# Kernel tuning notes

Hardware: AMD Instinct MI355X
Metric: run time of the kernel (lower is better)

The kernel has to match this reference:

```python
import jax, jax.numpy as jnp
import numpy as np

B, S, D, H = 4, 2048, 512, 8
DK = D // H
EPS = 1e-5


def setup_inputs() -> dict:
    key = jax.random.key(0)
    ks = jax.random.split(key, 9)
    inp = {
        "input_Q": jax.random.normal(ks[0], (B, S, D), jnp.float32),
        "input_K": jax.random.normal(ks[1], (B, S, D), jnp.float32),
        "input_V": jax.random.normal(ks[2], (B, S, D), jnp.float32),
        # causal mask: True = masked (upper triangle above diagonal)
        "attn_mask": jnp.broadcast_to(
            jnp.triu(jnp.ones((S, S), jnp.bool_), k=1), (B, S, S)
        ),
        # nn.Linear weights (torch stores [out, in]; y = x @ W.T)
        "Wq": jax.random.normal(ks[3], (D, D), jnp.float32) / np.sqrt(D),
        "Wk": jax.random.normal(ks[4], (D, D), jnp.float32) / np.sqrt(D),
        "Wv": jax.random.normal(ks[5], (D, D), jnp.float32) / np.sqrt(D),
        "Wo": jax.random.normal(ks[6], (D, D), jnp.float32) / np.sqrt(D),
        "gamma": jnp.ones((D,), jnp.float32),
        "beta": jnp.zeros((D,), jnp.float32),
    }
    return inp


def _layer_norm(x, gamma, beta):
    mu = jnp.mean(x, axis=-1, keepdims=True)
    var = jnp.mean(jnp.square(x - mu), axis=-1, keepdims=True)
    return (x - mu) * jax.lax.rsqrt(var + EPS) * gamma + beta


def reference(input_Q, input_K, input_V, attn_mask, Wq, Wk, Wv, Wo, gamma, beta):
    # projections: [B,S,D] -> [B,H,S,DK]
    def split_heads(x):
        return x.reshape(x.shape[0], x.shape[1], H, DK).transpose(0, 2, 1, 3)

    Q = split_heads(input_Q @ Wq.T)
    K = split_heads(input_K @ Wk.T)
    V = split_heads(input_V @ Wv.T)

    # scores: [B,H,Sq,Sk], explicit materialization as in the original
    scores = jnp.einsum("bhqd,bhkd->bhqk", Q, K) / np.sqrt(DK).astype(np.float32)
    scores = jnp.where(attn_mask[:, None, :, :], -jnp.inf, scores)
    attn = jax.nn.softmax(scores, axis=-1)
    context = jnp.einsum("bhqk,bhkd->bhqd", attn, V)  # [B,H,Sq,DK]

    context = context.transpose(0, 2, 1, 3).reshape(input_Q.shape[0], -1, D)
    output = context @ Wo.T
    out = _layer_norm(output + input_Q, gamma, beta)
    return (out, attn)
```

## Files before the change

kernel.cpp:

```cpp
#include <hip/hip_runtime.h>

typedef unsigned short u16;
typedef __bf16 bf16x8 __attribute__((ext_vector_type(8)));
typedef float f32x4 __attribute__((ext_vector_type(4)));
typedef unsigned short u16x4 __attribute__((ext_vector_type(4)));

#define MFMA_B16(a, b, c) __builtin_amdgcn_mfma_f32_16x16x32_bf16((a), (b), (c), 0, 0, 0)

__device__ __forceinline__ u16 f2bf(float f) {
  unsigned int u = __float_as_uint(f);
  u += 0x7FFFu + ((u >> 16) & 1u);
  return (u16)(u >> 16);
}

__device__ __forceinline__ u16x4 f4_to_bf4(float4 v) {
  u16x4 r;
  r[0] = f2bf(v.x); r[1] = f2bf(v.y); r[2] = f2bf(v.z); r[3] = f2bf(v.w);
  return r;
}

__global__ __launch_bounds__(256) void cvt3(const float* __restrict__ a,
                                            const float* __restrict__ b,
                                            const float* __restrict__ c,
                                            u16* __restrict__ dst, int n4, int n) {
  int i = blockIdx.x * 256 + threadIdx.x;
  int stride = gridDim.x * 256;
  const float4* a4 = (const float4*)a;
  const float4* b4 = (const float4*)b;
  const float4* c4 = (const float4*)c;
  u16x4* d0 = (u16x4*)dst;
  u16x4* d1 = (u16x4*)(dst + (size_t)n);
  u16x4* d2 = (u16x4*)(dst + (size_t)2 * n);
  for (; i < n4; i += stride) {
    d0[i] = f4_to_bf4(a4[i]);
    d1[i] = f4_to_bf4(b4[i]);
    d2[i] = f4_to_bf4(c4[i]);
  }
}

__global__ __launch_bounds__(256) void cvtW(const float* __restrict__ a,
                                            const float* __restrict__ b,
                                            const float* __restrict__ c,
                                            const float* __restrict__ d,
                                            u16* __restrict__ dst, int n4, int n) {
  int i = blockIdx.x * 256 + threadIdx.x;
  int stride = gridDim.x * 256;
  const float4* a4 = (const float4*)a;
  const float4* b4 = (const float4*)b;
  const float4* c4 = (const float4*)c;
  const float4* d4 = (const float4*)d;
  u16x4* o0 = (u16x4*)dst;
  u16x4* o1 = (u16x4*)(dst + (size_t)n);
  u16x4* o2 = (u16x4*)(dst + (size_t)2 * n);
  u16x4* o3 = (u16x4*)(dst + (size_t)3 * n);
  for (; i < n4; i += stride) {
    o0[i] = f4_to_bf4(a4[i]);
    o1[i] = f4_to_bf4(b4[i]);
    o2[i] = f4_to_bf4(c4[i]);
    o3[i] = f4_to_bf4(d4[i]);
  }
}

template <bool OUT_F32>
__device__ __forceinline__ void gemm_body(const u16* __restrict__ A,
                                          const u16* __restrict__ Bw,
                                          u16* __restrict__ Cb, float* __restrict__ Cf,
                                          int bm, int bn) {
  __shared__ __align__(16) u16 As[128][40];
  __shared__ __align__(16) u16 Bs[128][40];
  const int tid = threadIdx.x;
  const int wave = tid >> 6, lane = tid & 63;
  const int g = lane >> 4, l16 = lane & 15;
  const int wr = (wave >> 1) * 64, wc = (wave & 1) * 64;
  const int srow = tid >> 1, scol = (tid & 1) * 16;
  const u16* Ar = A + (size_t)(bm + srow) * 512 + scol;
  const u16* Br = Bw + (size_t)(bn + srow) * 512 + scol;
  f32x4 acc[4][4] = {};
  for (int k0 = 0; k0 < 512; k0 += 32) {
    *(uint4*)(&As[srow][scol])     = *(const uint4*)(Ar + k0);
    *(uint4*)(&As[srow][scol + 8]) = *(const uint4*)(Ar + k0 + 8);
    *(uint4*)(&Bs[srow][scol])     = *(const uint4*)(Br + k0);
    *(uint4*)(&Bs[srow][scol + 8]) = *(const uint4*)(Br + k0 + 8);
    __syncthreads();
    bf16x8 af[4], bfr[4];
#pragma unroll
    for (int i = 0; i < 4; ++i) af[i] = *(const bf16x8*)(&As[wr + i * 16 + l16][g * 8]);
#pragma unroll
    for (int j = 0; j < 4; ++j) bfr[j] = *(const bf16x8*)(&Bs[wc + j * 16 + l16][g * 8]);
#pragma unroll
    for (int i = 0; i < 4; ++i)
#pragma unroll
      for (int j = 0; j < 4; ++j)
        acc[i][j] = MFMA_B16(af[i], bfr[j], acc[i][j]);
    __syncthreads();
  }
#pragma unroll
  for (int i = 0; i < 4; ++i)
#pragma unroll
    for (int j = 0; j < 4; ++j)
#pragma unroll
      for (int r = 0; r < 4; ++r) {
        int row = bm + wr + i * 16 + g * 4 + r;
        int col = bn + wc + j * 16 + l16;
        if constexpr (OUT_F32)
          Cf[(size_t)row * 512 + col] = acc[i][j][r];
        else
          Cb[(size_t)row * 512 + col] = f2bf(acc[i][j][r]);
      }
}

__global__ __launch_bounds__(256) void gemm_qkv(const u16* __restrict__ Xbf,
                                                const u16* __restrict__ Wbf,
                                                u16* __restrict__ QKVp) {
  int z = blockIdx.z;
  gemm_body<false>(Xbf + (size_t)z * 4194304, Wbf + (size_t)z * 262144,
                   QKVp + (size_t)z * 4194304, nullptr,
                   blockIdx.x * 128, blockIdx.y * 128);
}

__global__ __launch_bounds__(256) void gemm_f32out(const u16* __restrict__ A,
                                                   const u16* __restrict__ Bw,
                                                   float* __restrict__ C) {
  gemm_body<true>(A, Bw, nullptr, C, blockIdx.x * 128, blockIdx.y * 128);
}

__global__ __launch_bounds__(256) void transpose_v(const u16* __restrict__ Vp,
                                                   u16* __restrict__ Vt) {
  __shared__ __align__(16) u16 t[64][72];
  const int b = blockIdx.z;
  const int s0 = blockIdx.x * 64, d0 = blockIdx.y * 64;
  const u16* in = Vp + (size_t)b * 2048 * 512;
  u16* outp = Vt + (size_t)b * 512 * 2048;
  const int tid = threadIdx.x;
  const int r = tid >> 2;
  const int c = (tid & 3) * 16;
  const uint4* src = (const uint4*)(in + (size_t)(s0 + r) * 512 + d0 + c);
  uint4 v0 = src[0], v1 = src[1];
  *(uint4*)(&t[r][c]) = v0;
  *(uint4*)(&t[r][c + 8]) = v1;
  __syncthreads();
  u16 tmp[16];
#pragma unroll
  for (int j = 0; j < 16; ++j) tmp[j] = t[c + j][r];
  uint4* dst = (uint4*)(outp + (size_t)(d0 + r) * 2048 + s0 + c);
  dst[0] = *(uint4*)(&tmp[0]);
  dst[1] = *(uint4*)(&tmp[8]);
}

__global__ __launch_bounds__(512, 2) void lsum_kernel(const u16* __restrict__ Qp,
                                                      const u16* __restrict__ Kp,
                                                      float* __restrict__ invl) {
  __shared__ __align__(16) u16 Ks[2][8192];
  const int tid = threadIdx.x;
  const int wave = tid >> 6, lane = tid & 63;
  const int g = lane >> 4, l16 = lane & 15;
  const int id = blockIdx.x;
  const int xcd = id & 7;
  const int r = id >> 3;
  const int bh = xcd * 4 + (r & 3);
  const int p = r >> 2;
  const int strip = wave >> 2;
  const int pw = wave & 3;
  const int nktH = 16 - p, nktL = p + 1;
  const int myNkt = strip ? nktL : nktH;
  const int myBase = (strip ? p : 15 - p) * 128 + pw * 32;
  const int b = bh >> 3, h = bh & 7;
  const char* KhB = (const char*)Kp + (size_t)b * 2097152 + h * 128;
  const u16* Qh = Qp + (size_t)b * 1048576 + h * 64;
  char* KsC = (char*)Ks;

  const int sr_r = tid >> 2;
  const int sr_c = (tid & 3) * 2;
  const size_t sr_src = (size_t)sr_r * 1024 + sr_c * 16;
  const int sr_d0 = sr_r * 128 + ((sr_c ^ (sr_r & 7)) << 4);
  const int sr_d1 = sr_r * 128 + (((sr_c + 1) ^ (sr_r & 7)) << 4);
  uint4 sr[2];

#define STAGE_LOAD(KT)                                                         \
  { sr[0] = *(const uint4*)(KhB + (size_t)(KT) * 131072 + sr_src);             \
    sr[1] = *(const uint4*)(KhB + (size_t)(KT) * 131072 + sr_src + 16); }
#define STAGE_WRITE(CUR)                                                       \
  { *(uint4*)(KsC + (CUR) * 16384 + sr_d0) = sr[0];                            \
    *(uint4*)(KsC + (CUR) * 16384 + sr_d1) = sr[1]; }
#define BAR_READS_DONE()                                                       \
  { asm volatile("" ::: "memory");                                             \
    __builtin_amdgcn_s_barrier();                                              \
    __builtin_amdgcn_sched_barrier(0); }
#define BAR_WRITES_VISIBLE()                                                   \
  { asm volatile("s_waitcnt lgkmcnt(0)" ::: "memory");                         \
    __builtin_amdgcn_sched_barrier(0);                                         \
    __builtin_amdgcn_s_barrier();                                              \
    __builtin_amdgcn_sched_barrier(0); }

  const int qrow0 = myBase + l16;
  const int qrow1 = myBase + 16 + l16;
  bf16x8 q00 = *(const bf16x8*)(Qh + (size_t)qrow0 * 512 + g * 8);
  bf16x8 q01 = *(const bf16x8*)(Qh + (size_t)qrow0 * 512 + 32 + g * 8);
  bf16x8 q10 = *(const bf16x8*)(Qh + (size_t)qrow1 * 512 + g * 8);
  bf16x8 q11 = *(const bf16x8*)(Qh + (size_t)qrow1 * 512 + 32 + g * 8);

  float ls0 = 0.f, ls1 = 0.f;
  STAGE_LOAD(0); STAGE_WRITE(0);
  if (nktH > 1) STAGE_LOAD(1);
  BAR_WRITES_VISIBLE();
  int cur = 0;
  for (int kt = 0; kt < nktH; ++kt) {
    const int ktb = kt * 128;
    const bool act = (kt < myNkt);
    const bool dg = (kt == myNkt - 1);
    const char* Kc = KsC + cur * 16384;
    if (act) {
#pragma unroll
      for (int kf = 0; kf < 8; ++kf) {
        const int ro = (kf * 16 + l16) * 128;
        bf16x8 ka = *(const bf16x8*)(Kc + ro + ((g ^ (l16 & 7)) << 4));
        bf16x8 kb = *(const bf16x8*)(Kc + ro + (((4 + g) ^ (l16 & 7)) << 4));
        const int kbase = ktb + kf * 16 + g * 4;
        f32x4 c0 = {0.f, 0.f, 0.f, 0.f};
        f32x4 c1 = {0.f, 0.f, 0.f, 0.f};
        __builtin_amdgcn_s_setprio(1);
        c0 = MFMA_B16(ka, q00, c0);
        c0 = MFMA_B16(kb, q01, c0);
        c1 = MFMA_B16(ka, q10, c1);
        c1 = MFMA_B16(kb, q11, c1);
        __builtin_amdgcn_s_setprio(0);
        if (dg) {
#pragma unroll
          for (int rr = 0; rr < 4; ++rr) {
            ls0 += (kbase + rr > qrow0) ? 0.f : __expf(c0[rr] * 0.125f);
            ls1 += (kbase + rr > qrow1) ? 0.f : __expf(c1[rr] * 0.125f);
          }
        } else {
          ls0 += __expf(c0[0] * 0.125f) + __expf(c0[1] * 0.125f)
               + __expf(c0[2] * 0.125f) + __expf(c0[3] * 0.125f);
          ls1 += __expf(c1[0] * 0.125f) + __expf(c1[1] * 0.125f)
               + __expf(c1[2] * 0.125f) + __expf(c1[3] * 0.125f);
        }
      }
    }
    if (kt + 1 < nktH) {
      BAR_READS_DONE();
      STAGE_WRITE(cur ^ 1);
      if (kt + 2 < nktH) STAGE_LOAD(kt + 2);
      BAR_WRITES_VISIBLE();
      cur ^= 1;
    }
  }
  ls0 += __shfl_xor(ls0, 16); ls0 += __shfl_xor(ls0, 32);
  ls1 += __shfl_xor(ls1, 16); ls1 += __shfl_xor(ls1, 32);
  if (lane < 16) {
    invl[(size_t)bh * 2048 + qrow0] = 1.f / ls0;
    invl[(size_t)bh * 2048 + qrow1] = 1.f / ls1;
  }
#undef STAGE_LOAD
#undef STAGE_WRITE
#undef BAR_READS_DONE
#undef BAR_WRITES_VISIBLE
}

__global__ __launch_bounds__(512, 4) void attn_kernel(const u16* __restrict__ Qp,
                                                      const u16* __restrict__ Kp,
                                                      const u16* __restrict__ Vt,
                                                      const float* __restrict__ invl,
                                                      float* __restrict__ attn_all,
                                                      u16* __restrict__ ctx) {
  __shared__ __align__(16) u16 Ks[2][8192];
  __shared__ __align__(16) u16 Plds[8][16][128];
  const int tid = threadIdx.x;
  const int wave = tid >> 6, lane = tid & 63;
  const int g = lane >> 4, l16 = lane & 15;
  const int strip = wave >> 2;
  const int pw = wave & 3;
  const int id = blockIdx.x;
  const int r8 = id >> 3;
  const int bh = (id & 7) * 4 + (r8 & 3);
  const int pair = r8 >> 2;
  const int sLo = pair, sHi = 31 - pair;
  const int b = bh >> 3, h = bh & 7;
  const int nktH = sHi / 2 + 1, nktL = sLo / 2 + 1;
  const int myNkt = strip ? nktL : nktH;
  const int myS = strip ? sLo : sHi;
  const char* KhB = (const char*)Kp + (size_t)b * 2097152 + h * 128;
  const char* VhB = (const char*)Vt + ((size_t)b * 512 + h * 64) * 4096;
  const u16* Qh = Qp + (size_t)b * 1048576 + h * 64;
  float* attn = attn_all + (size_t)bh * 4194304;
  char* KsC = (char*)Ks;
  char* Pw = (char*)&Plds[wave][0][0];
  const int swk = (l16 & 7) << 4;

  const int sr_r = tid >> 2;
  const int sr_c = (tid & 3) * 2;
  const size_t sr_src = (size_t)sr_r * 1024 + sr_c * 16;
  const int sr_d0 = sr_r * 128 + ((sr_c ^ (sr_r & 7)) << 4);
  const int sr_d1 = sr_r * 128 + (((sr_c + 1) ^ (sr_r & 7)) << 4);
  uint4 sr[2];

#define STAGE_LOAD(KT)                                                         \
  { sr[0] = *(const uint4*)(KhB + (size_t)(KT) * 131072 + sr_src);             \
    sr[1] = *(const uint4*)(KhB + (size_t)(KT) * 131072 + sr_src + 16); }
#define STAGE_WRITE(CUR)                                                       \
  { *(uint4*)(KsC + (CUR) * 16384 + sr_d0) = sr[0];                            \
    *(uint4*)(KsC + (CUR) * 16384 + sr_d1) = sr[1]; }
#define BAR_READS_DONE()                                                       \
  { asm volatile("" ::: "memory");                                             \
    __builtin_amdgcn_s_barrier();                                              \
    __builtin_amdgcn_sched_barrier(0); }
#define BAR_WRITES_VISIBLE()                                                   \
  { asm volatile("s_waitcnt lgkmcnt(0)" ::: "memory");                         \
    __builtin_amdgcn_sched_barrier(0);                                         \
    __builtin_amdgcn_s_barrier();                                              \
    __builtin_amdgcn_sched_barrier(0); }

  const int qr = myS * 64 + pw * 16;
  const int qrow = qr + l16;

  bf16x8 q0 = *(const bf16x8*)(Qh + (size_t)qrow * 512 + g * 8);
  bf16x8 q1 = *(const bf16x8*)(Qh + (size_t)qrow * 512 + 32 + g * 8);
  const float inv = invl[(size_t)bh * 2048 + qrow];

  f32x4 oacc[4] = {};
  {
    STAGE_LOAD(0); STAGE_WRITE(0);
    if (nktH > 1) STAGE_LOAD(1);
    BAR_WRITES_VISIBLE();
    int cur = 0;
    for (int kt = 0; kt < nktH; ++kt) {
      const int ktb = kt * 128;
      const bool act = (kt < myNkt);
      const bool dg = (kt == myNkt - 1);
      const char* Kc = KsC + cur * 16384;
      if (act) {
#pragma unroll
        for (int kf = 0; kf < 8; ++kf) {
          const int ro = (kf * 16 + l16) * 128;
          bf16x8 ka = *(const bf16x8*)(Kc + ro + ((g ^ (l16 & 7)) << 4));
          bf16x8 kb = *(const bf16x8*)(Kc + ro + (((4 + g) ^ (l16 & 7)) << 4));
          const int kbase = ktb + kf * 16 + g * 4;
          f32x4 c = {0.f, 0.f, 0.f, 0.f};
          __builtin_amdgcn_s_setprio(1);
          c = MFMA_B16(ka, q0, c);
          c = MFMA_B16(kb, q1, c);
          __builtin_amdgcn_s_setprio(0);
          float p[4];
#pragma unroll
          for (int r = 0; r < 4; ++r) {
            float e = __expf(c[r] * 0.125f) * inv;
            p[r] = (dg && (kbase + r > qrow)) ? 0.f : e;
          }
          unsigned lo = (unsigned)f2bf(p[0]) | ((unsigned)f2bf(p[1]) << 16);
          unsigned hi = (unsigned)f2bf(p[2]) | ((unsigned)f2bf(p[3]) << 16);
          *(uint2*)(Pw + l16 * 256 + ((kf * 32 + g * 8) ^ swk)) = make_uint2(lo, hi);
        }
#pragma unroll
        for (int kb4 = 0; kb4 < 4; ++kb4) {
          bf16x8 pa = *(const bf16x8*)(Pw + l16 * 256 + ((kb4 * 64 + g * 16) ^ swk));
#pragma unroll
          for (int cn = 0; cn < 4; ++cn) {
            bf16x8 vb = *(const bf16x8*)(VhB + (size_t)(cn * 16 + l16) * 4096 +
                                         (ktb + kb4 * 32 + g * 8) * 2);
            __builtin_amdgcn_s_setprio(1);
            oacc[cn] = MFMA_B16(pa, vb, oacc[cn]);
            __builtin_amdgcn_s_setprio(0);
          }
        }
        {
          const int c32 = lane & 31;
          const int rh = lane >> 5;
#pragma unroll
          for (int i = 0; i < 8; ++i) {
            const int row = i * 2 + rh;
            uint2 pk = *(const uint2*)(Pw + row * 256 + ((c32 * 8) ^ ((row & 7) << 4)));
            f32x4 o;
            o[0] = __uint_as_float(pk.x << 16);
            o[1] = __uint_as_float(pk.x & 0xffff0000u);
            o[2] = __uint_as_float(pk.y << 16);
            o[3] = __uint_as_float(pk.y & 0xffff0000u);
            __builtin_nontemporal_store(o, (f32x4*)(&attn[(size_t)(qr + row) * 2048 + ktb + c32 * 4]));
          }
        }
      }
      if (kt + 1 < nktH) {
        BAR_READS_DONE();
        STAGE_WRITE(cur ^ 1);
        if (kt + 2 < nktH) STAGE_LOAD(kt + 2);
        BAR_WRITES_VISIBLE();
        cur ^= 1;
      }
    }
  }

  u16* cb = ctx + (size_t)b * 1048576 + h * 64;
#pragma unroll
  for (int cn = 0; cn < 4; ++cn)
#pragma unroll
    for (int r = 0; r < 4; ++r)
      cb[(size_t)(qr + g * 4 + r) * 512 + cn * 16 + l16] = f2bf(oacc[cn][r]);

  {
    const int base = myS * 64;
    const int z0 = myNkt * 128;
    f32x4 z4 = {0.f, 0.f, 0.f, 0.f};
    if (z0 < 2048) {
      for (int r = pw; r < 64; r += 4) {
        float* rowp = attn + (size_t)(base + r) * 2048;
        for (int c = z0 + lane * 4; c < 2048; c += 256)
          __builtin_nontemporal_store(z4, (f32x4*)(rowp + c));
      }
    }
  }
#undef STAGE_LOAD
#undef STAGE_WRITE
#undef BAR_READS_DONE
#undef BAR_WRITES_VISIBLE
}

__global__ __launch_bounds__(256) void ln_kernel(const float* __restrict__ proj,
                                                 const float* __restrict__ resid,
                                                 const float* __restrict__ gamma,
                                                 const float* __restrict__ beta,
                                                 float* __restrict__ out) {
  const int wave = threadIdx.x >> 6, lane = threadIdx.x & 63;
  const int row = blockIdx.x * 4 + wave;
  const float4* p4 = (const float4*)(proj + (size_t)row * 512);
  const float4* r4 = (const float4*)(resid + (size_t)row * 512);
  float4 a0 = p4[lane * 2], a1 = p4[lane * 2 + 1];
  float4 q0 = r4[lane * 2], q1 = r4[lane * 2 + 1];
  float x[8];
  x[0] = a0.x + q0.x; x[1] = a0.y + q0.y; x[2] = a0.z + q0.z; x[3] = a0.w + q0.w;
  x[4] = a1.x + q1.x; x[5] = a1.y + q1.y; x[6] = a1.z + q1.z; x[7] = a1.w + q1.w;
  float s = 0.f;
#pragma unroll
  for (int j = 0; j < 8; ++j) s += x[j];
#pragma unroll
  for (int d = 1; d < 64; d <<= 1) s += __shfl_xor(s, d);
  float mu = s * (1.f / 512.f);
  float v = 0.f;
#pragma unroll
  for (int j = 0; j < 8; ++j) { float t = x[j] - mu; v += t * t; }
#pragma unroll
  for (int d = 1; d < 64; d <<= 1) v += __shfl_xor(v, d);
  float rs = rsqrtf(v * (1.f / 512.f) + 1e-5f);
  const float4* g4 = (const float4*)gamma;
  const float4* b4 = (const float4*)beta;
  float4 g0 = g4[lane * 2], g1 = g4[lane * 2 + 1];
  float4 bb0 = b4[lane * 2], bb1 = b4[lane * 2 + 1];
  float4 y0, y1;
  y0.x = (x[0] - mu) * rs * g0.x + bb0.x;
  y0.y = (x[1] - mu) * rs * g0.y + bb0.y;
  y0.z = (x[2] - mu) * rs * g0.z + bb0.z;
  y0.w = (x[3] - mu) * rs * g0.w + bb0.w;
  y1.x = (x[4] - mu) * rs * g1.x + bb1.x;
  y1.y = (x[5] - mu) * rs * g1.y + bb1.y;
  y1.z = (x[6] - mu) * rs * g1.z + bb1.z;
  y1.w = (x[7] - mu) * rs * g1.w + bb1.w;
  float4* o4 = (float4*)(out + (size_t)row * 512);
  o4[lane * 2] = y0;
  o4[lane * 2 + 1] = y1;
}

extern "C" void kernel_launch(void* const* d_in, const int* in_sizes, int n_in,
                              void* d_out, int out_size, void* d_ws, size_t ws_size,
                              hipStream_t stream) {
  (void)in_sizes; (void)n_in; (void)out_size; (void)ws_size;
  const float* inQ = (const float*)d_in[0];
  const float* inK = (const float*)d_in[1];
  const float* inV = (const float*)d_in[2];
  const float* Wq = (const float*)d_in[4];
  const float* Wk = (const float*)d_in[5];
  const float* Wv = (const float*)d_in[6];
  const float* Wo = (const float*)d_in[7];
  const float* gamma = (const float*)d_in[8];
  const float* beta = (const float*)d_in[9];

  float* out = (float*)d_out;
  float* attn = out + (size_t)4 * 2048 * 512;

  char* ws = (char*)d_ws;
  u16* Qp  = (u16*)(ws + 0);
  u16* Kp  = (u16*)(ws + 8388608);
  u16* Vp  = (u16*)(ws + 16777216);
  u16* Vt  = (u16*)(ws + 25165824);
  u16* ctx = (u16*)(ws + 33554432);
  u16* Wbf = (u16*)(ws + 41943040);
  float* invl = (float*)(ws + 16777216);
  float* proj = (float*)(ws + 0);
  u16* Xbf = (u16*)attn;

  cvt3<<<2048, 256, 0, stream>>>(inQ, inK, inV, Xbf, 1048576, 4194304);
  cvtW<<<256, 256, 0, stream>>>(Wq, Wk, Wv, Wo, Wbf, 65536, 262144);
  gemm_qkv<<<dim3(64, 4, 3), 256, 0, stream>>>(Xbf, Wbf, Qp);
  transpose_v<<<dim3(32, 8, 4), 256, 0, stream>>>(Vp, Vt);
  lsum_kernel<<<256, 512, 0, stream>>>(Qp, Kp, invl);
  attn_kernel<<<dim3(512), 512, 0, stream>>>(Qp, Kp, Vt, invl, attn, ctx);
  gemm_f32out<<<dim3(64, 4, 1), 256, 0, stream>>>(ctx, Wbf + (size_t)3 * 262144, proj);
  ln_kernel<<<2048, 256, 0, stream>>>(proj, inQ, gamma, beta, out);
}
```

Measured before the change: 268.0 us.

## Use direct global-to-LDS loads with XOR swizzle in GEMMs; fuse residual add

The GEMM tile loads now use global_load_lds to write straight into shared memory instead of staging through registers. The padded LDS layout is replaced by an XOR-swizzled one so fragment reads stay free of bank conflicts. The residual add moves from the layernorm kernel into the output-projection epilogue, which removes one full read pass in the LN kernel. The residual read in the epilogue is strided per element rather than vectorised, which may offset part of that saving.

```diff
diff --git a/kernel.cpp b/kernel.cpp
--- a/kernel.cpp
+++ b/kernel.cpp
@@ -17,6 +17,12 @@
   u16x4 r;
   r[0] = f2bf(v.x); r[1] = f2bf(v.y); r[2] = f2bf(v.z); r[3] = f2bf(v.w);
   return r;
+}
+
+__device__ __forceinline__ void gl_lds16(const u16* g, u16* l) {
+  __builtin_amdgcn_global_load_lds(
+      (const __attribute__((address_space(1))) void*)g,
+      (__attribute__((address_space(3))) void*)l, 16, 0, 0);
 }
 
 __global__ __launch_bounds__(256) void cvt3(const float* __restrict__ a,
@@ -65,28 +71,46 @@
 __device__ __forceinline__ void gemm_body(const u16* __restrict__ A,
                                           const u16* __restrict__ Bw,
                                           u16* __restrict__ Cb, float* __restrict__ Cf,
+                                          const float* __restrict__ resid,
                                           int bm, int bn) {
-  __shared__ __align__(16) u16 As[128][40];
-  __shared__ __align__(16) u16 Bs[128][40];
+  __shared__ __align__(16) u16 As[128 * 32];
+  __shared__ __align__(16) u16 Bs[128 * 32];
   const int tid = threadIdx.x;
   const int wave = tid >> 6, lane = tid & 63;
   const int g = lane >> 4, l16 = lane & 15;
   const int wr = (wave >> 1) * 64, wc = (wave & 1) * 64;
-  const int srow = tid >> 1, scol = (tid & 1) * 16;
-  const u16* Ar = A + (size_t)(bm + srow) * 512 + scol;
-  const u16* Br = Bw + (size_t)(bn + srow) * 512 + scol;
+
+  const int r0 = wave * 32 + (lane >> 2);
+  const int r1 = r0 + 16;
+  const int c0 = (((lane & 3) ^ ((r0 >> 1) & 3)) << 3);
+  const int c1 = (((lane & 3) ^ ((r1 >> 1) & 3)) << 3);
+  const u16* Ar0 = A + (size_t)(bm + r0) * 512 + c0;
+  const u16* Ar1 = A + (size_t)(bm + r1) * 512 + c1;
+  const u16* Br0 = Bw + (size_t)(bn + r0) * 512 + c0;
+  const u16* Br1 = Bw + (size_t)(bn + r1) * 512 + c1;
+  u16* Ad0 = As + (wave * 32) * 32;
+  u16* Ad1 = As + (wave * 32 + 16) * 32;
+  u16* Bd0 = Bs + (wave * 32) * 32;
+  u16* Bd1 = Bs + (wave * 32 + 16) * 32;
+
   f32x4 acc[4][4] = {};
   for (int k0 = 0; k0 < 512; k0 += 32) {
-    *(uint4*)(&As[srow][scol])     = *(const uint4*)(Ar + k0);
-    *(uint4*)(&As[srow][scol + 8]) = *(const uint4*)(Ar + k0 + 8);
-    *(uint4*)(&Bs[srow][scol])     = *(const uint4*)(Br + k0);
-    *(uint4*)(&Bs[srow][scol + 8]) = *(const uint4*)(Br + k0 + 8);
+    gl_lds16(Ar0 + k0, Ad0);
+    gl_lds16(Ar1 + k0, Ad1);
+    gl_lds16(Br0 + k0, Bd0);
+    gl_lds16(Br1 + k0, Bd1);
     __syncthreads();
     bf16x8 af[4], bfr[4];
 #pragma unroll
-    for (int i = 0; i < 4; ++i) af[i] = *(const bf16x8*)(&As[wr + i * 16 + l16][g * 8]);
-#pragma unroll
-    for (int j = 0; j < 4; ++j) bfr[j] = *(const bf16x8*)(&Bs[wc + j * 16 + l16][g * 8]);
+    for (int i = 0; i < 4; ++i) {
+      const int ar = wr + i * 16 + l16;
+      af[i] = *(const bf16x8*)((const char*)As + ar * 64 + ((g ^ ((ar >> 1) & 3)) << 4));
+    }
+#pragma unroll
+    for (int j = 0; j < 4; ++j) {
+      const int br = wc + j * 16 + l16;
+      bfr[j] = *(const bf16x8*)((const char*)Bs + br * 64 + ((g ^ ((br >> 1) & 3)) << 4));
+    }
 #pragma unroll
     for (int i = 0; i < 4; ++i)
 #pragma unroll
@@ -103,7 +127,7 @@
         int row = bm + wr + i * 16 + g * 4 + r;
         int col = bn + wc + j * 16 + l16;
         if constexpr (OUT_F32)
-          Cf[(size_t)row * 512 + col] = acc[i][j][r];
+          Cf[(size_t)row * 512 + col] = acc[i][j][r] + resid[(size_t)row * 512 + col];
         else
           Cb[(size_t)row * 512 + col] = f2bf(acc[i][j][r]);
       }
@@ -114,14 +138,15 @@
                                                 u16* __restrict__ QKVp) {
   int z = blockIdx.z;
   gemm_body<false>(Xbf + (size_t)z * 4194304, Wbf + (size_t)z * 262144,
-                   QKVp + (size_t)z * 4194304, nullptr,
+                   QKVp + (size_t)z * 4194304, nullptr, nullptr,
                    blockIdx.x * 128, blockIdx.y * 128);
 }
 
 __global__ __launch_bounds__(256) void gemm_f32out(const u16* __restrict__ A,
                                                    const u16* __restrict__ Bw,
-                                                   float* __restrict__ C) {
-  gemm_body<true>(A, Bw, nullptr, C, blockIdx.x * 128, blockIdx.y * 128);
+                                                   float* __restrict__ C,
+                                                   const float* __restrict__ resid) {
+  gemm_body<true>(A, Bw, nullptr, C, resid, blockIdx.x * 128, blockIdx.y * 128);
 }
 
 __global__ __launch_bounds__(256) void transpose_v(const u16* __restrict__ Vp,
@@ -415,19 +440,16 @@
 }
 
 __global__ __launch_bounds__(256) void ln_kernel(const float* __restrict__ proj,
-                                                 const float* __restrict__ resid,
                                                  const float* __restrict__ gamma,
                                                  const float* __restrict__ beta,
                                                  float* __restrict__ out) {
   const int wave = threadIdx.x >> 6, lane = threadIdx.x & 63;
   const int row = blockIdx.x * 4 + wave;
   const float4* p4 = (const float4*)(proj + (size_t)row * 512);
-  const float4* r4 = (const float4*)(resid + (size_t)row * 512);
   float4 a0 = p4[lane * 2], a1 = p4[lane * 2 + 1];
-  float4 q0 = r4[lane * 2], q1 = r4[lane * 2 + 1];
   float x[8];
-  x[0] = a0.x + q0.x; x[1] = a0.y + q0.y; x[2] = a0.z + q0.z; x[3] = a0.w + q0.w;
-  x[4] = a1.x + q1.x; x[5] = a1.y + q1.y; x[6] = a1.z + q1.z; x[7] = a1.w + q1.w;
+  x[0] = a0.x; x[1] = a0.y; x[2] = a0.z; x[3] = a0.w;
+  x[4] = a1.x; x[5] = a1.y; x[6] = a1.z; x[7] = a1.w;
   float s = 0.f;
 #pragma unroll
   for (int j = 0; j < 8; ++j) s += x[j];
@@ -492,6 +514,6 @@
   transpose_v<<<dim3(32, 8, 4), 256, 0, stream>>>(Vp, Vt);
   lsum_kernel<<<256, 512, 0, stream>>>(Qp, Kp, invl);
   attn_kernel<<<dim3(512), 512, 0, stream>>>(Qp, Kp, Vt, invl, attn, ctx);
-  gemm_f32out<<<dim3(64, 4, 1), 256, 0, stream>>>(ctx, Wbf + (size_t)3 * 262144, proj);
-  ln_kernel<<<2048, 256, 0, stream>>>(proj, inQ, gamma, beta, out);
-}
+  gemm_f32out<<<dim3(64, 4, 1), 256, 0, stream>>>(ctx, Wbf + (size_t)3 * 262144, proj, inQ);
+  ln_kernel<<<2048, 256, 0, stream>>>(proj, gamma, beta, out);
+}
```

Measured after the change: 261.3 us. 2.5% less time.
